# Performance work log

Hardware: AMD Instinct MI355X
Metric: run time of the kernel (lower is better)

The kernel has to match this reference:

```python
import jax, jax.numpy as jnp
import numpy as np

D, H, E, K, S = 1024, 2048, 8, 2, 1  # dim, expert hidden, n_experts, top_k, n_shared
B, L = 4, 2048


def setup_inputs() -> dict:
    key = jax.random.key(0)
    ks = jax.random.split(key, 9)
    std = 0.02
    return {
        "x": jax.random.normal(ks[0], (B, L, D), dtype=jnp.float32),
        "router_w": jax.random.normal(ks[1], (E, D), dtype=jnp.float32) * std,
        "experts_bias": jnp.zeros((E,), dtype=jnp.float32),  # aux-free LB bias buffer
        "w1": jax.random.normal(ks[2], (E, D, H), dtype=jnp.float32) * std,
        "w3": jax.random.normal(ks[3], (E, D, H), dtype=jnp.float32) * std,
        "w2": jax.random.normal(ks[4], (E, H, D), dtype=jnp.float32) * std,
        "sw1": jax.random.normal(ks[5], (S, D, H), dtype=jnp.float32) * std,
        "sw3": jax.random.normal(ks[6], (S, D, H), dtype=jnp.float32) * std,
        "sw2": jax.random.normal(ks[7], (S, H, D), dtype=jnp.float32) * std,
    }


def reference(x, router_w, experts_bias, w1, w3, w2, sw1, sw3, sw2):
    b, l, d = x.shape
    xf = x.reshape(-1, d)  # [T, D], T = b*l

    # shared experts (SwiGLU FFN), summed over S
    sg = jnp.einsum("td,sdh->tsh", xf, sw1)
    su = jnp.einsum("td,sdh->tsh", xf, sw3)
    shared_out = jnp.einsum("tsh,shd->td", jax.nn.silu(sg) * su, sw2)

    # router + aux-free load-balancing bias
    logits = xf @ router_w.T + experts_bias  # [T, E]
    rw, sel = jax.lax.top_k(logits, K)       # [T, K]
    rw = jax.nn.softmax(rw.astype(jnp.float32), axis=-1).astype(x.dtype)

    # combine weights scattered to [T, E]; equals torch one_hot dispatch+index_add
    cw = (jax.nn.one_hot(sel, E, dtype=x.dtype) * rw[..., None]).sum(axis=1)

    # all-expert SwiGLU, weighted-combined (identical math: unselected weight = 0)
    g = jnp.einsum("td,edh->teh", xf, w1)
    u = jnp.einsum("td,edh->teh", xf, w3)
    eo = jax.nn.silu(g) * u  # [T, E, H]
    moe_out = jnp.einsum("te,teh,ehd->td", cw, eo, w2)

    return (moe_out + shared_out).reshape(b, l, d)
```

## Files before the change

kernel.cpp:

```cpp
#include <hip/hip_runtime.h>
#include <stdint.h>

#define T_TOK 8192
#define DIMV  1024
#define HIDV  2048
#define NE    8
#define CAP   8192
#define ASSIGN_TOT 24576

typedef __attribute__((ext_vector_type(8))) short          bf16x8;
typedef __attribute__((ext_vector_type(4))) float          floatx4;

__device__ __forceinline__ unsigned short f2bf(float f) {
    union { float f; unsigned int i; } v; v.f = f;
    unsigned int i = v.i;
    return (unsigned short)((i + 0x7FFFu + ((i >> 16) & 1u)) >> 16);
}

__device__ __forceinline__ void gll16(const void* g, void* l) {
    __builtin_amdgcn_global_load_lds((const __attribute__((address_space(1))) void*)g,
                                     (__attribute__((address_space(3))) void*)l,
                                     16, 0, 0);
}

__global__ __launch_bounds__(256) void xconv_kernel(
    const float* __restrict__ src, unsigned short* __restrict__ dst)
{
    size_t i = ((size_t)blockIdx.x * 256 + threadIdx.x) * 4;
    float4 v = *(const float4*)(src + i);
    ushort4 o;
    o.x = f2bf(v.x); o.y = f2bf(v.y); o.z = f2bf(v.z); o.w = f2bf(v.w);
    *(ushort4*)(dst + i) = o;
}

__global__ __launch_bounds__(256) void router_kernel(
    const float* __restrict__ x,
    const float* __restrict__ rwp,
    const float* __restrict__ biasp,
    int* __restrict__ cnt, int* __restrict__ tlist, float* __restrict__ wlist)
{
    const int t    = blockIdx.x * 4 + (threadIdx.x >> 6);
    const int lane = threadIdx.x & 63;
    const float* xr = x + (size_t)t * DIMV + lane * 16;
    float xf[16];
#pragma unroll
    for (int q = 0; q < 4; q++) {
        float4 v = *(const float4*)(xr + q * 4);
        xf[q*4+0] = v.x; xf[q*4+1] = v.y; xf[q*4+2] = v.z; xf[q*4+3] = v.w;
    }
    float acc[NE];
#pragma unroll
    for (int e = 0; e < NE; e++) {
        const float* wr = rwp + (size_t)e * DIMV + lane * 16;
        float s = 0.f;
#pragma unroll
        for (int q = 0; q < 4; q++) {
            float4 v = *(const float4*)(wr + q * 4);
            s += xf[q*4+0]*v.x + xf[q*4+1]*v.y + xf[q*4+2]*v.z + xf[q*4+3]*v.w;
        }
        acc[e] = s;
    }
#pragma unroll
    for (int e = 0; e < NE; e++)
#pragma unroll
        for (int off = 32; off; off >>= 1) acc[e] += __shfl_xor(acc[e], off, 64);

    if (lane == 0) {
        float lg[NE];
#pragma unroll
        for (int e = 0; e < NE; e++) lg[e] = acc[e] + biasp[e];
        int e0 = 0;
#pragma unroll
        for (int e = 1; e < NE; e++) if (lg[e] > lg[e0]) e0 = e;
        int e1 = (e0 == 0) ? 1 : 0;
#pragma unroll
        for (int e = 0; e < NE; e++) if (e != e0 && lg[e] > lg[e1]) e1 = e;
        float z  = __expf(lg[e1] - lg[e0]);
        float p0 = 1.f / (1.f + z);
        float p1 = z  / (1.f + z);
        int s0 = atomicAdd(cnt + e0, 1);
        tlist[e0 * CAP + s0] = t; wlist[e0 * CAP + s0] = p0;
        int s1 = atomicAdd(cnt + e1, 1);
        tlist[e1 * CAP + s1] = t; wlist[e1 * CAP + s1] = p1;
    }
}

__global__ void offsets_kernel(const int* __restrict__ cnt, int* __restrict__ goff)
{
    if (threadIdx.x == 0 && blockIdx.x == 0) {
        int s = 0;
        for (int e = 0; e < NE; e++) { goff[e] = s; s += cnt[e]; }
        goff[NE] = 16384;
    }
}

__global__ __launch_bounds__(256) void ctrans_kernel(
    const float* __restrict__ src, unsigned short* __restrict__ dst,
    int R, int C)
{
    __shared__ unsigned short tile[64][65];
    const size_t mo = (size_t)blockIdx.z * R * C;
    const int c0 = blockIdx.x * 64, r0 = blockIdx.y * 64;
    const int cc = threadIdx.x & 63, rr = threadIdx.x >> 6;
#pragma unroll
    for (int i = 0; i < 16; i++) {
        int r = rr * 16 + i;
        tile[r][cc] = f2bf(src[mo + (size_t)(r0 + r) * C + (c0 + cc)]);
    }
    __syncthreads();
#pragma unroll
    for (int i = 0; i < 16; i++) {
        int c = rr * 16 + i;
        dst[mo + (size_t)(c0 + c) * R + (r0 + cc)] = tile[cc][c];
    }
}

__global__ __launch_bounds__(256, 2) void up_gemm(
    const unsigned short* __restrict__ x,
    const unsigned short* __restrict__ w1t,
    const unsigned short* __restrict__ w3t,
    const unsigned short* __restrict__ sw1t,
    const unsigned short* __restrict__ sw3t,
    const int* __restrict__ cnt, const int* __restrict__ goff,
    const int* __restrict__ tlist,
    unsigned short* __restrict__ hbuf)
{
    const int g = blockIdx.z;
    int n_rows, row_off;
    const unsigned short *B1p, *B3p;
    if (g < NE) {
        n_rows = cnt[g]; row_off = goff[g];
        B1p = w1t + (size_t)g * HIDV * DIMV;
        B3p = w3t + (size_t)g * HIDV * DIMV;
    } else {
        n_rows = T_TOK; row_off = 16384;
        B1p = sw1t; B3p = sw3t;
    }
    const int m0 = blockIdx.y * 128;
    if (m0 >= n_rows) return;
    const int n0 = blockIdx.x * 64;

    __shared__ __align__(16) unsigned short Al[128 * 32];
    __shared__ __align__(16) unsigned short B1l[64 * 32];
    __shared__ __align__(16) unsigned short B3l[64 * 32];

    const int tid  = threadIdx.x;
    const int lane = tid & 63;
    const int wave = tid >> 6;
    const int r0   = tid >> 2;
    const int ck   = tid & 3;

    int tokA, tokB;
    if (g < NE) {
        int ra = m0 + r0, rb = m0 + 64 + r0;
        tokA = (ra < n_rows) ? tlist[g * CAP + ra] : 0;
        tokB = (rb < n_rows) ? tlist[g * CAP + rb] : 0;
    } else { tokA = m0 + r0; tokB = m0 + 64 + r0; }

    const unsigned short* gA0 = x + (size_t)tokA * DIMV + ck * 8;
    const unsigned short* gA1 = x + (size_t)tokB * DIMV + ck * 8;
    const unsigned short* gB1 = B1p + (size_t)(n0 + r0) * DIMV + ck * 8;
    const unsigned short* gB3 = B3p + (size_t)(n0 + r0) * DIMV + ck * 8;

    char* AlB0 = (char*)Al  + wave * 1024;
    char* AlB1 = (char*)Al  + 4096 + wave * 1024;
    char* B1B  = (char*)B1l + wave * 1024;
    char* B3B  = (char*)B3l + wave * 1024;

    const int wm = wave & 1, wn = wave >> 1;
    const int m16 = lane & 15, quad = lane >> 4;

    floatx4 accg[4][2] = {};
    floatx4 accu[4][2] = {};

    const unsigned short* Afp  = Al  + (wm * 64 + m16) * 32 + quad * 8;
    const unsigned short* B1fp = B1l + (wn * 32 + m16) * 32 + quad * 8;
    const unsigned short* B3fp = B3l + (wn * 32 + m16) * 32 + quad * 8;

    for (int k0 = 0; k0 < DIMV; k0 += 32) {
        __syncthreads();
        gll16(gA0 + k0, AlB0);
        gll16(gA1 + k0, AlB1);
        gll16(gB1 + k0, B1B);
        gll16(gB3 + k0, B3B);
        __syncthreads();
        bf16x8 af[4], b1f[2], b3f[2];
#pragma unroll
        for (int i = 0; i < 4; i++) af[i] = *(const bf16x8*)(Afp + i * 16 * 32);
#pragma unroll
        for (int j = 0; j < 2; j++) {
            b1f[j] = *(const bf16x8*)(B1fp + j * 16 * 32);
            b3f[j] = *(const bf16x8*)(B3fp + j * 16 * 32);
        }
#pragma unroll
        for (int i = 0; i < 4; i++)
#pragma unroll
            for (int j = 0; j < 2; j++) {
                accg[i][j] = __builtin_amdgcn_mfma_f32_16x16x32_bf16(af[i], b1f[j], accg[i][j], 0, 0, 0);
                accu[i][j] = __builtin_amdgcn_mfma_f32_16x16x32_bf16(af[i], b3f[j], accu[i][j], 0, 0, 0);
            }
    }

#pragma unroll
    for (int i = 0; i < 4; i++) {
#pragma unroll
        for (int ii = 0; ii < 4; ii++) {
            int r = m0 + wm * 64 + i * 16 + quad * 4 + ii;
            if (r < n_rows) {
#pragma unroll
                for (int j = 0; j < 2; j++) {
                    int col = n0 + wn * 32 + j * 16 + m16;
                    float gv = accg[i][j][ii], uv = accu[i][j][ii];
                    float s  = gv / (1.0f + __expf(-gv));
                    hbuf[(size_t)(row_off + r) * HIDV + col] = f2bf(s * uv);
                }
            }
        }
    }
}

__global__ __launch_bounds__(256, 2) void down_gemm(
    const unsigned short* __restrict__ hbuf,
    const unsigned short* __restrict__ w2t,
    const unsigned short* __restrict__ sw2t,
    const int* __restrict__ cnt, const int* __restrict__ goff,
    const int* __restrict__ tlist, const float* __restrict__ wlist,
    float* __restrict__ outp, int gbase)
{
    const int g = gbase + blockIdx.z;
    int n_rows, row_off;
    const unsigned short* Bp;
    if (g < NE) {
        n_rows = cnt[g]; row_off = goff[g];
        Bp = w2t + (size_t)g * DIMV * HIDV;
    } else {
        n_rows = T_TOK; row_off = 16384;
        Bp = sw2t;
    }
    const int m0 = blockIdx.y * 128;
    if (m0 >= n_rows) return;
    const int n0 = blockIdx.x * 64;

    __shared__ __align__(16) unsigned short Al[128 * 32];
    __shared__ __align__(16) unsigned short Bl[64 * 32];

    const int tid  = threadIdx.x;
    const int lane = tid & 63;
    const int wave = tid >> 6;
    const int r0   = tid >> 2;
    const int ck   = tid & 3;

    const unsigned short* gA0 = hbuf + (size_t)(row_off + m0 + r0) * HIDV + ck * 8;
    const unsigned short* gA1 = hbuf + (size_t)(row_off + m0 + 64 + r0) * HIDV + ck * 8;
    const unsigned short* gB  = Bp + (size_t)(n0 + r0) * HIDV + ck * 8;

    char* AlB0 = (char*)Al + wave * 1024;
    char* AlB1 = (char*)Al + 4096 + wave * 1024;
    char* BB   = (char*)Bl + wave * 1024;

    const int wm = wave & 1, wn = wave >> 1;
    const int m16 = lane & 15, quad = lane >> 4;

    floatx4 acc[4][2] = {};

    const unsigned short* Afp = Al + (wm * 64 + m16) * 32 + quad * 8;
    const unsigned short* Bfp = Bl + (wn * 32 + m16) * 32 + quad * 8;

    for (int k0 = 0; k0 < HIDV; k0 += 32) {
        __syncthreads();
        gll16(gA0 + k0, AlB0);
        gll16(gA1 + k0, AlB1);
        gll16(gB  + k0, BB);
        __syncthreads();
        bf16x8 af[4], bf[2];
#pragma unroll
        for (int i = 0; i < 4; i++) af[i] = *(const bf16x8*)(Afp + i * 16 * 32);
#pragma unroll
        for (int j = 0; j < 2; j++) bf[j] = *(const bf16x8*)(Bfp + j * 16 * 32);
#pragma unroll
        for (int i = 0; i < 4; i++)
#pragma unroll
            for (int j = 0; j < 2; j++)
                acc[i][j] = __builtin_amdgcn_mfma_f32_16x16x32_bf16(af[i], bf[j], acc[i][j], 0, 0, 0);
    }

#pragma unroll
    for (int i = 0; i < 4; i++) {
#pragma unroll
        for (int ii = 0; ii < 4; ii++) {
            int r = m0 + wm * 64 + i * 16 + quad * 4 + ii;
            if (r < n_rows) {
                int tok; float wgt;
                if (g < NE) { tok = tlist[g * CAP + r]; wgt = wlist[g * CAP + r]; }
                else        { tok = r;                  wgt = 1.0f; }
#pragma unroll
                for (int j = 0; j < 2; j++) {
                    int col = n0 + wn * 32 + j * 16 + m16;
                    float v = acc[i][j][ii] * wgt;
                    if (g < NE) atomicAdd(outp + (size_t)tok * DIMV + col, v);
                    else        outp[(size_t)tok * DIMV + col] = v;
                }
            }
        }
    }
}

extern "C" void kernel_launch(void* const* d_in, const int* in_sizes, int n_in,
                              void* d_out, int out_size, void* d_ws, size_t ws_size,
                              hipStream_t stream)
{
    (void)in_sizes; (void)n_in; (void)out_size; (void)ws_size;
    const float* x    = (const float*)d_in[0];
    const float* rw   = (const float*)d_in[1];
    const float* bias = (const float*)d_in[2];
    const float* w1   = (const float*)d_in[3];
    const float* w3   = (const float*)d_in[4];
    const float* w2   = (const float*)d_in[5];
    const float* sw1  = (const float*)d_in[6];
    const float* sw3  = (const float*)d_in[7];
    const float* sw2  = (const float*)d_in[8];
    float* outp = (float*)d_out;

    char* p = (char*)d_ws;
    auto alloc = [&](size_t b) { char* r = p; p += (b + 255) & ~(size_t)255; return r; };
    int*   cnt   = (int*)  alloc(64);
    int*   goffp = (int*)  alloc(64);
    int*   tlist = (int*)  alloc((size_t)NE * CAP * 4);
    float* wlist = (float*)alloc((size_t)NE * CAP * 4);
    unsigned short* xb   = (unsigned short*)alloc((size_t)T_TOK * DIMV * 2);
    unsigned short* hbuf = (unsigned short*)alloc((size_t)ASSIGN_TOT * HIDV * 2);
    unsigned short* w1t  = (unsigned short*)alloc((size_t)NE * HIDV * DIMV * 2);
    unsigned short* w3t  = (unsigned short*)alloc((size_t)NE * HIDV * DIMV * 2);
    unsigned short* w2t  = (unsigned short*)alloc((size_t)NE * DIMV * HIDV * 2);
    unsigned short* sw1t = (unsigned short*)alloc((size_t)HIDV * DIMV * 2);
    unsigned short* sw3t = (unsigned short*)alloc((size_t)HIDV * DIMV * 2);
    unsigned short* sw2t = (unsigned short*)alloc((size_t)DIMV * HIDV * 2);

    hipMemsetAsync(cnt, 0, 64, stream);

    dim3 blk(256);
    xconv_kernel<<<dim3((T_TOK * DIMV) / 1024), blk, 0, stream>>>(x, xb);
    ctrans_kernel<<<dim3(HIDV/64, DIMV/64, NE), blk, 0, stream>>>(w1, w1t, DIMV, HIDV);
    ctrans_kernel<<<dim3(HIDV/64, DIMV/64, NE), blk, 0, stream>>>(w3, w3t, DIMV, HIDV);
    ctrans_kernel<<<dim3(DIMV/64, HIDV/64, NE), blk, 0, stream>>>(w2, w2t, HIDV, DIMV);
    ctrans_kernel<<<dim3(HIDV/64, DIMV/64, 1),  blk, 0, stream>>>(sw1, sw1t, DIMV, HIDV);
    ctrans_kernel<<<dim3(HIDV/64, DIMV/64, 1),  blk, 0, stream>>>(sw3, sw3t, DIMV, HIDV);
    ctrans_kernel<<<dim3(DIMV/64, HIDV/64, 1),  blk, 0, stream>>>(sw2, sw2t, HIDV, DIMV);

    router_kernel<<<dim3(T_TOK/4), blk, 0, stream>>>(x, rw, bias, cnt, tlist, wlist);
    offsets_kernel<<<dim3(1), dim3(64), 0, stream>>>(cnt, goffp);

    up_gemm<<<dim3(HIDV/64, 64, 9), blk, 0, stream>>>(xb, w1t, w3t, sw1t, sw3t,
                                                      cnt, goffp, tlist, hbuf);
    down_gemm<<<dim3(DIMV/64, 64, 1), blk, 0, stream>>>(hbuf, w2t, sw2t, cnt, goffp,
                                                        tlist, wlist, outp, 8);
    down_gemm<<<dim3(DIMV/64, 64, 8), blk, 0, stream>>>(hbuf, w2t, sw2t, cnt, goffp,
                                                        tlist, wlist, outp, 0);
}
```

Before: 933.6 us.

## Fuse x conversion into router, vectorize and merge weight transposes, swizzle GEMM LDS

The fp32-to-bf16 conversion of x moves into the router kernel, which already reads x, so one full pass over the activations is removed. The six weight-transpose launches become two batched kernels using float4 loads and 16-byte stores instead of scalar accesses. Both GEMMs apply an XOR swizzle to the 16-byte chunk index on the global-to-LDS load and on the fragment read, to reduce LDS bank conflicts. Fewer launches and wider memory transactions target the preprocessing cost. The swizzle has to match exactly on the write and read sides or the results will be wrong.

```diff
diff --git a/kernel.cpp b/kernel.cpp
--- a/kernel.cpp
+++ b/kernel.cpp
@@ -9,6 +9,7 @@
 #define ASSIGN_TOT 24576
 
 typedef __attribute__((ext_vector_type(8))) short          bf16x8;
+typedef __attribute__((ext_vector_type(8))) unsigned short u16x8;
 typedef __attribute__((ext_vector_type(4))) float          floatx4;
 
 __device__ __forceinline__ unsigned short f2bf(float f) {
@@ -23,20 +24,11 @@
                                      16, 0, 0);
 }
 
-__global__ __launch_bounds__(256) void xconv_kernel(
-    const float* __restrict__ src, unsigned short* __restrict__ dst)
-{
-    size_t i = ((size_t)blockIdx.x * 256 + threadIdx.x) * 4;
-    float4 v = *(const float4*)(src + i);
-    ushort4 o;
-    o.x = f2bf(v.x); o.y = f2bf(v.y); o.z = f2bf(v.z); o.w = f2bf(v.w);
-    *(ushort4*)(dst + i) = o;
-}
-
 __global__ __launch_bounds__(256) void router_kernel(
     const float* __restrict__ x,
     const float* __restrict__ rwp,
     const float* __restrict__ biasp,
+    unsigned short* __restrict__ xb,
     int* __restrict__ cnt, int* __restrict__ tlist, float* __restrict__ wlist)
 {
     const int t    = blockIdx.x * 4 + (threadIdx.x >> 6);
@@ -47,6 +39,14 @@
     for (int q = 0; q < 4; q++) {
         float4 v = *(const float4*)(xr + q * 4);
         xf[q*4+0] = v.x; xf[q*4+1] = v.y; xf[q*4+2] = v.z; xf[q*4+3] = v.w;
+    }
+    {
+        u16x8 o0, o1;
+#pragma unroll
+        for (int j = 0; j < 8; j++) { o0[j] = f2bf(xf[j]); o1[j] = f2bf(xf[8 + j]); }
+        unsigned short* xo = xb + (size_t)t * DIMV + lane * 16;
+        *(u16x8*)xo = o0;
+        *(u16x8*)(xo + 8) = o1;
     }
     float acc[NE];
 #pragma unroll
@@ -94,25 +94,61 @@
     }
 }
 
-__global__ __launch_bounds__(256) void ctrans_kernel(
-    const float* __restrict__ src, unsigned short* __restrict__ dst,
-    int R, int C)
-{
-    __shared__ unsigned short tile[64][65];
-    const size_t mo = (size_t)blockIdx.z * R * C;
+template<int R, int C>
+__device__ __forceinline__ void ctrans_body(
+    const float* __restrict__ src, unsigned short* __restrict__ dstp,
+    unsigned short (*tile)[66])
+{
     const int c0 = blockIdx.x * 64, r0 = blockIdx.y * 64;
-    const int cc = threadIdx.x & 63, rr = threadIdx.x >> 6;
-#pragma unroll
-    for (int i = 0; i < 16; i++) {
-        int r = rr * 16 + i;
-        tile[r][cc] = f2bf(src[mo + (size_t)(r0 + r) * C + (c0 + cc)]);
+    const int tid = threadIdx.x;
+    const int lr = tid >> 4;
+    const int lc = (tid & 15) * 4;
+#pragma unroll
+    for (int i = 0; i < 4; i++) {
+        int r = lr + 16 * i;
+        float4 v = *(const float4*)(src + (size_t)(r0 + r) * C + (c0 + lc));
+        ushort4 o; o.x = f2bf(v.x); o.y = f2bf(v.y); o.z = f2bf(v.z); o.w = f2bf(v.w);
+        *(ushort4*)&tile[r][lc] = o;
     }
     __syncthreads();
-#pragma unroll
-    for (int i = 0; i < 16; i++) {
-        int c = rr * 16 + i;
-        dst[mo + (size_t)(c0 + c) * R + (r0 + cc)] = tile[cc][c];
-    }
+    const int oc  = tid >> 3;
+    const int orr = (tid & 7) * 8;
+#pragma unroll
+    for (int i = 0; i < 2; i++) {
+        int c = oc + 32 * i;
+        u16x8 tmp;
+#pragma unroll
+        for (int j = 0; j < 8; j++) tmp[j] = tile[orr + j][c];
+        *(u16x8*)(dstp + (size_t)(c0 + c) * R + (r0 + orr)) = tmp;
+    }
+}
+
+__global__ __launch_bounds__(256) void ctransA_kernel(
+    const float* __restrict__ w1, const float* __restrict__ w3,
+    const float* __restrict__ sw1, const float* __restrict__ sw3,
+    unsigned short* __restrict__ w1t, unsigned short* __restrict__ w3t,
+    unsigned short* __restrict__ sw1t, unsigned short* __restrict__ sw3t)
+{
+    __shared__ unsigned short tile[64][66];
+    const int z = blockIdx.z;
+    const float* src; unsigned short* dstp;
+    if (z < 8)       { src = w1  + (size_t)z * DIMV * HIDV;      dstp = w1t + (size_t)z * DIMV * HIDV; }
+    else if (z < 16) { src = w3  + (size_t)(z - 8) * DIMV * HIDV; dstp = w3t + (size_t)(z - 8) * DIMV * HIDV; }
+    else if (z == 16){ src = sw1; dstp = sw1t; }
+    else             { src = sw3; dstp = sw3t; }
+    ctrans_body<DIMV, HIDV>(src, dstp, tile);
+}
+
+__global__ __launch_bounds__(256) void ctransB_kernel(
+    const float* __restrict__ w2, const float* __restrict__ sw2,
+    unsigned short* __restrict__ w2t, unsigned short* __restrict__ sw2t)
+{
+    __shared__ unsigned short tile[64][66];
+    const int z = blockIdx.z;
+    const float* src; unsigned short* dstp;
+    if (z < 8) { src = w2 + (size_t)z * HIDV * DIMV; dstp = w2t + (size_t)z * HIDV * DIMV; }
+    else       { src = sw2; dstp = sw2t; }
+    ctrans_body<HIDV, DIMV>(src, dstp, tile);
 }
 
 __global__ __launch_bounds__(256, 2) void up_gemm(
@@ -148,7 +184,7 @@
     const int lane = tid & 63;
     const int wave = tid >> 6;
     const int r0   = tid >> 2;
-    const int ck   = tid & 3;
+    const int ck   = (tid & 3) ^ ((r0 >> 1) & 3);
 
     int tokA, tokB;
     if (g < NE) {
@@ -169,13 +205,14 @@
 
     const int wm = wave & 1, wn = wave >> 1;
     const int m16 = lane & 15, quad = lane >> 4;
+    const int sw  = (m16 >> 1) & 3;
 
     floatx4 accg[4][2] = {};
     floatx4 accu[4][2] = {};
 
-    const unsigned short* Afp  = Al  + (wm * 64 + m16) * 32 + quad * 8;
-    const unsigned short* B1fp = B1l + (wn * 32 + m16) * 32 + quad * 8;
-    const unsigned short* B3fp = B3l + (wn * 32 + m16) * 32 + quad * 8;
+    const unsigned short* Afp  = Al  + (wm * 64 + m16) * 32 + (quad ^ sw) * 8;
+    const unsigned short* B1fp = B1l + (wn * 32 + m16) * 32 + (quad ^ sw) * 8;
+    const unsigned short* B3fp = B3l + (wn * 32 + m16) * 32 + (quad ^ sw) * 8;
 
     for (int k0 = 0; k0 < DIMV; k0 += 32) {
         __syncthreads();
@@ -248,7 +285,7 @@
     const int lane = tid & 63;
     const int wave = tid >> 6;
     const int r0   = tid >> 2;
-    const int ck   = tid & 3;
+    const int ck   = (tid & 3) ^ ((r0 >> 1) & 3);
 
     const unsigned short* gA0 = hbuf + (size_t)(row_off + m0 + r0) * HIDV + ck * 8;
     const unsigned short* gA1 = hbuf + (size_t)(row_off + m0 + 64 + r0) * HIDV + ck * 8;
@@ -260,11 +297,12 @@
 
     const int wm = wave & 1, wn = wave >> 1;
     const int m16 = lane & 15, quad = lane >> 4;
+    const int sw  = (m16 >> 1) & 3;
 
     floatx4 acc[4][2] = {};
 
-    const unsigned short* Afp = Al + (wm * 64 + m16) * 32 + quad * 8;
-    const unsigned short* Bfp = Bl + (wn * 32 + m16) * 32 + quad * 8;
+    const unsigned short* Afp = Al + (wm * 64 + m16) * 32 + (quad ^ sw) * 8;
+    const unsigned short* Bfp = Bl + (wn * 32 + m16) * 32 + (quad ^ sw) * 8;
 
     for (int k0 = 0; k0 < HIDV; k0 += 32) {
         __syncthreads();
@@ -339,15 +377,10 @@
     hipMemsetAsync(cnt, 0, 64, stream);
 
     dim3 blk(256);
-    xconv_kernel<<<dim3((T_TOK * DIMV) / 1024), blk, 0, stream>>>(x, xb);
-    ctrans_kernel<<<dim3(HIDV/64, DIMV/64, NE), blk, 0, stream>>>(w1, w1t, DIMV, HIDV);
-    ctrans_kernel<<<dim3(HIDV/64, DIMV/64, NE), blk, 0, stream>>>(w3, w3t, DIMV, HIDV);
-    ctrans_kernel<<<dim3(DIMV/64, HIDV/64, NE), blk, 0, stream>>>(w2, w2t, HIDV, DIMV);
-    ctrans_kernel<<<dim3(HIDV/64, DIMV/64, 1),  blk, 0, stream>>>(sw1, sw1t, DIMV, HIDV);
-    ctrans_kernel<<<dim3(HIDV/64, DIMV/64, 1),  blk, 0, stream>>>(sw3, sw3t, DIMV, HIDV);
-    ctrans_kernel<<<dim3(DIMV/64, HIDV/64, 1),  blk, 0, stream>>>(sw2, sw2t, HIDV, DIMV);
-
-    router_kernel<<<dim3(T_TOK/4), blk, 0, stream>>>(x, rw, bias, cnt, tlist, wlist);
+    router_kernel<<<dim3(T_TOK/4), blk, 0, stream>>>(x, rw, bias, xb, cnt, tlist, wlist);
+    ctransA_kernel<<<dim3(HIDV/64, DIMV/64, 18), blk, 0, stream>>>(w1, w3, sw1, sw3,
+                                                                   w1t, w3t, sw1t, sw3t);
+    ctransB_kernel<<<dim3(DIMV/64, HIDV/64, 9),  blk, 0, stream>>>(w2, sw2, w2t, sw2t);
     offsets_kernel<<<dim3(1), dim3(64), 0, stream>>>(cnt, goffp);
 
     up_gemm<<<dim3(HIDV/64, 64, 9), blk, 0, stream>>>(xb, w1t, w3t, sw1t, sw3t,
```

Result: faster. 901.2 us (-3.5%).
